# Performance work log

Hardware: AMD Instinct MI355X
Metric: run time of the kernel (lower is better)

The kernel has to match this reference:

```python
import jax, jax.numpy as jnp
import numpy as np

IH = IW = 1024          # image size (iH, iW)
NMS_CAND = 1000         # dup_attrs['nms_candidates']
NMS_THR = 0.65          # dup_attrs['nms_thr']
MAX_SEGS = 100          # max_segs


def _mask_to_box(masks):
    # masks: [N, H, W] bool -> xyxy float boxes [N, 4] in pixel coords
    N, H, W = masks.shape
    rows = masks.any(axis=2)            # [N, H]
    cols = masks.any(axis=1)            # [N, W]
    x1 = jnp.argmax(cols, axis=1)
    x2 = W - jnp.argmax(cols[:, ::-1], axis=1)
    y1 = jnp.argmax(rows, axis=1)
    y2 = H - jnp.argmax(rows[:, ::-1], axis=1)
    return jnp.stack([x1, y1, x2, y2], axis=-1).astype(jnp.float32)


def _box_iou(b):
    # b: [K, 4] xyxy -> pairwise IoU [K, K]
    x1, y1, x2, y2 = b[:, 0], b[:, 1], b[:, 2], b[:, 3]
    area = (x2 - x1) * (y2 - y1)
    ix1 = jnp.maximum(x1[:, None], x1[None, :])
    iy1 = jnp.maximum(y1[:, None], y1[None, :])
    ix2 = jnp.minimum(x2[:, None], x2[None, :])
    iy2 = jnp.minimum(y2[:, None], y2[None, :])
    inter = jnp.clip(ix2 - ix1, 0.0) * jnp.clip(iy2 - iy1, 0.0)
    union = area[:, None] + area[None, :] - inter
    return inter / jnp.maximum(union, 1e-9)


def _greedy_nms_keep(iou, thr):
    # boxes assumed pre-sorted by descending score; returns keep mask [K]
    k = iou.shape[0]
    idx = jnp.arange(k)

    def body(i, keep):
        sup = keep[i] & (iou[i] > thr) & (idx > i)
        return keep & ~sup

    return jax.lax.fori_loop(0, k, body, jnp.ones((k,), dtype=bool))


def setup_inputs() -> dict:
    key = jax.random.key(0)
    k1, k2 = jax.random.split(key)
    cls_logits = jax.random.normal(k1, (300, 81), dtype=jnp.float32)
    seg_logits = jax.random.normal(k2, (300, 200, 200), dtype=jnp.float32)
    return {"cls_logits": cls_logits, "seg_logits": seg_logits}


def reference(cls_logits, seg_logits):
    N, fH, fW = seg_logits.shape
    C = cls_logits.shape[1] - 1  # last class is background/no-object

    # mask thresholding + emptiness flag (filtering replaced by score masking)
    pred_masks = seg_logits > 0                              # [N, fH, fW]
    non_empty = pred_masks.reshape(N, -1).sum(axis=1) > 0    # [N]

    # mask -> box for NMS
    boxes = _mask_to_box(pred_masks)                         # [N, 4]

    # sigmoid scoring over (feat, class); empty masks get score -1 (never picked)
    scores = jax.nn.sigmoid(cls_logits[:, :-1])              # [N, C]
    scores = jnp.where(non_empty[:, None], scores, -1.0).reshape(-1)  # [N*C]
    feat_ids = jnp.repeat(jnp.arange(N), C)                  # [N*C]
    labels = jnp.tile(jnp.arange(C), N)                      # [N*C]

    # top nms_candidates (scores sorted descending)
    k = min(NMS_CAND, N * C)
    cand_scores, cand_ids = jax.lax.top_k(scores, k)
    cand_feats = feat_ids[cand_ids]
    cand_labels = labels[cand_ids]
    cand_boxes = boxes[cand_feats]

    # batched (class-aware) NMS: offset boxes per label
    offset = cand_labels.astype(jnp.float32)[:, None] * (float(max(fH, fW)) + 1.0)
    iou = _box_iou(cand_boxes + offset)
    keep = _greedy_nms_keep(iou, NMS_THR) & (cand_scores >= 0.0)

    # keep top max_segs among survivors
    kept_scores = jnp.where(keep, cand_scores, -jnp.inf)
    sel_scores, sel = jax.lax.top_k(kept_scores, MAX_SEGS)
    sel_feats = cand_feats[sel]
    sel_labels = cand_labels[sel]

    # upsample selected mask logits to image size and threshold
    sel_logits = seg_logits[sel_feats]                       # [M, fH, fW]
    maps = jax.image.resize(sel_logits, (MAX_SEGS, IH, IW), method='bilinear')
    out_masks = maps > 0                                     # [M, iH, iW] bool
    batch_ids = jnp.zeros((MAX_SEGS,), dtype=jnp.int32)

    return sel_labels, out_masks, sel_scores, batch_ids
```

## Files before the change

### kernel.cpp

```cpp
#include <hip/hip_runtime.h>
#include <cstdint>
#include <cstddef>

typedef unsigned int u32;
typedef unsigned long long u64;
typedef float vf4 __attribute__((ext_vector_type(4)));

#define NF 300
#define NCLS 80
#define NCLS1 81
#define FH 200
#define FW 200
#define PIX 40000
#define NC 24000
#define KCAND 1000
#define CAP 4096
#define NBINS 65536
#define MAXSEG 100
#define OUT_MASK_OFF 100
#define OUT_SCORE_OFF 104857700
#define OUT_BATCH_OFF 104857800
#define NEG_BIG -3.3895313892515355e38f
#define RYC 8

#define WS_HIST      0u
#define WS_KEYS      262144u
#define WS_COLLECT   454144u
#define WS_CNT       486912u
#define WS_BOXES     486928u
#define WS_CLAB      496928u
#define WS_CFEAT     500928u
#define WS_CSCORE    504928u
#define WS_CBOX      508928u
#define WS_ROWBITS   524928u
#define WS_SELFEAT   656128u
#define WS_WTAB      656528u

__device__ __forceinline__ u32 ord32_r3(float f) {
  u32 b = __float_as_uint(f);
  return (b & 0x80000000u) ? ~b : (b | 0x80000000u);
}
__device__ __forceinline__ float unord32_r3(u32 o) {
  u32 b = (o & 0x80000000u) ? (o & 0x7FFFFFFFu) : ~o;
  return __uint_as_float(b);
}

__global__ void r3_init_wtab(u32* __restrict__ hist, u32* __restrict__ cnts,
                             float4* __restrict__ wtab) {
  int i = blockIdx.x * 256 + threadIdx.x;
  hist[i] = 0u;
  if (i < 4) cnts[i] = 0u;
  if (i < 1024) {
    float s = __fsub_rn(__fmul_rn((float)i + 0.5f, 0.1953125f), 0.5f);
    int j0 = (int)floorf(s);
    int j1 = j0 + 1;
    float w0 = fmaxf(0.f, __fsub_rn(1.f, fabsf(__fsub_rn(s, (float)j0))));
    float w1 = fmaxf(0.f, __fsub_rn(1.f, fabsf(__fsub_rn(s, (float)j1))));
    bool in0 = (j0 >= 0) && (j0 < FH);
    bool in1 = (j1 >= 0) && (j1 < FH);
    float tot = __fadd_rn(in0 ? w0 : 0.f, in1 ? w1 : 0.f);
    float w0n = in0 ? (w0 / tot) : 0.f;
    float w1n = in1 ? (w1 / tot) : 0.f;
    wtab[i] = make_float4(w0n, w1n, (float)max(j0, 0), (float)min(j1, FH - 1));
  }
}

__global__ void r3_boxes_scores(const float* __restrict__ seg, const float* __restrict__ cls,
                                float4* __restrict__ boxes, u64* __restrict__ keys,
                                u32* __restrict__ hist) {
  __shared__ int sminx[256], sminy[256], smaxx[256], smaxy[256];
  int n = blockIdx.x, t = threadIdx.x;
  const float4* img = (const float4*)(seg + (size_t)n * PIX);
  int minx = FW, miny = FH, maxx = -1, maxy = -1;
  for (int q = t; q < PIX / 4; q += 256) {
    float4 v = img[q];
    int p = q * 4;
    int y = p / FW;
    int x = p - y * FW;
    if (v.x > 0.f) { minx = min(minx, x);     maxx = max(maxx, x);     miny = min(miny, y); maxy = max(maxy, y); }
    if (v.y > 0.f) { minx = min(minx, x + 1); maxx = max(maxx, x + 1); miny = min(miny, y); maxy = max(maxy, y); }
    if (v.z > 0.f) { minx = min(minx, x + 2); maxx = max(maxx, x + 2); miny = min(miny, y); maxy = max(maxy, y); }
    if (v.w > 0.f) { minx = min(minx, x + 3); maxx = max(maxx, x + 3); miny = min(miny, y); maxy = max(maxy, y); }
  }
  sminx[t] = minx; sminy[t] = miny; smaxx[t] = maxx; smaxy[t] = maxy;
  __syncthreads();
  for (int s = 128; s > 0; s >>= 1) {
    if (t < s) {
      sminx[t] = min(sminx[t], sminx[t + s]);
      sminy[t] = min(sminy[t], sminy[t + s]);
      smaxx[t] = max(smaxx[t], smaxx[t + s]);
      smaxy[t] = max(smaxy[t], smaxy[t + s]);
    }
    __syncthreads();
  }
  bool ne = smaxx[0] >= 0;
  if (t == 0) {
    float4 b;
    if (ne) b = make_float4((float)sminx[0], (float)sminy[0], (float)(smaxx[0] + 1), (float)(smaxy[0] + 1));
    else    b = make_float4(0.f, 0.f, (float)FW, (float)FH);
    boxes[n] = b;
  }
  if (t < NCLS) {
    float sc;
    if (ne) {
      float lg = cls[n * NCLS1 + t];
      sc = 1.0f / (1.0f + expf(-lg));
    } else {
      sc = -1.0f;
    }
    u32 o = ord32_r3(sc);
    u32 i = (u32)(n * NCLS + t);
    keys[i] = ((u64)o << 32) | (u64)(0xFFFFFFFFu - i);
    atomicAdd(&hist[o >> 16], 1u);
  }
}

__global__ void r3_thresh(const u32* __restrict__ hist, u32* __restrict__ cnts) {
  __shared__ u32 s[1024];
  int t = threadIdx.x;
  u32 sum = 0;
  const u32* hp = hist + t * 64;
  for (int b = 0; b < 64; b++) sum += hp[b];
  s[t] = sum;
  __syncthreads();
  for (int off = 1; off < 1024; off <<= 1) {
    u32 v = s[t];
    u32 o = (t + off < 1024) ? s[t + off] : 0u;
    __syncthreads();
    s[t] = v + o;
    __syncthreads();
  }
  u32 sufnext = (t < 1023) ? s[t + 1] : 0u;
  if (s[t] >= (u32)KCAND && sufnext < (u32)KCAND) {
    u32 run = sufnext;
    u32 B = (u32)(t * 64);
    for (int b = 63; b >= 0; b--) {
      run += hist[t * 64 + b];
      if (run >= (u32)KCAND) { B = (u32)(t * 64 + b); break; }
    }
    cnts[1] = B;
  }
}

__global__ void r3_collect(const u64* __restrict__ keys, const u32* __restrict__ cnts,
                           u64* __restrict__ collect, u32* __restrict__ counter) {
  int i = blockIdx.x * 256 + threadIdx.x;
  if (i >= NC) return;
  u64 k = keys[i];
  if ((u32)(k >> 48) >= cnts[1]) {
    u32 pos = atomicAdd(counter, 1u);
    if (pos < CAP) collect[pos] = k;
  }
}

__global__ void r3_rank(const u64* __restrict__ collect, const u32* __restrict__ cnts,
                        const float4* __restrict__ boxes,
                        int* __restrict__ clab, int* __restrict__ cfeat,
                        float* __restrict__ cscore, float4* __restrict__ cbox) {
  __shared__ u64 sk[CAP];
  int M = min((int)cnts[0], CAP);
  int t = threadIdx.x;
  for (int j = t; j < M; j += 64) sk[j] = collect[j];
  __syncthreads();
  for (int j = blockIdx.x * 64 + t; j < M; j += 64 * 16) {
    u64 mykey = sk[j];
    int r = 0;
    for (int k = 0; k < M; k++) r += (sk[k] > mykey) ? 1 : 0;
    if (r < KCAND) {
      u32 idx = 0xFFFFFFFFu - (u32)(mykey & 0xFFFFFFFFull);
      int n = (int)idx / NCLS, c = (int)idx - n * NCLS;
      clab[r] = c;
      cfeat[r] = n;
      cscore[r] = unord32_r3((u32)(mykey >> 32));
      float4 b = boxes[n];
      float off = (float)c * 201.0f;
      cbox[r] = make_float4(b.x + off, b.y + off, b.z + off, b.w + off);
    }
  }
}

__global__ void r3_iou(const float4* __restrict__ cbox, u64* __restrict__ rowbits) {
  int i = blockIdx.x;
  int lane = threadIdx.x;
  float4 bi = make_float4(0.f, 0.f, 0.f, 0.f);
  float ai = 0.f;
  if (i < KCAND) { bi = cbox[i]; ai = (bi.z - bi.x) * (bi.w - bi.y); }
  for (int ch = 0; ch < 16; ch++) {
    int j = ch * 64 + lane;
    bool pred = false;
    if (i < KCAND && j < KCAND && j > i) {
      float4 bj = cbox[j];
      float aj = (bj.z - bj.x) * (bj.w - bj.y);
      float ix1 = fmaxf(bi.x, bj.x), iy1 = fmaxf(bi.y, bj.y);
      float ix2 = fminf(bi.z, bj.z), iy2 = fminf(bi.w, bj.w);
      float inter = fmaxf(ix2 - ix1, 0.f) * fmaxf(iy2 - iy1, 0.f);
      float uni = ai + aj - inter;
      float iou = inter / fmaxf(uni, 1e-9f);
      pred = iou > 0.65f;
    }
    u64 m = __ballot(pred);
    if (lane == 0) rowbits[(size_t)i * 16 + ch] = m;
  }
}

__global__ void r3_nms_sel(const u64* __restrict__ rowbits, const float* __restrict__ cscore,
                           const int* __restrict__ clab, const int* __restrict__ cfeat,
                           float* __restrict__ out, int* __restrict__ selfeat) {
  __shared__ u64 sup[16];
  __shared__ u64 keep[16];
  __shared__ u64 sk[KCAND];
  int t = threadIdx.x;
  if (t < 16) sup[t] = 0ull;
  __syncthreads();
  for (int c = 0; c < 16; c++) {
    if (t < 64) {
      int L = t;
      u64 r = rowbits[(size_t)(c * 64 + L) * 16 + c];
      u64 s = sup[c];
      u64 k = 0ull;
      #pragma unroll 4
      for (int b = 0; b < 64; b++) {
        u64 rb = __shfl(r, b, 64);
        if (!((s >> b) & 1ull)) { s |= rb; k |= (1ull << b); }
      }
      if (L == 0) { sup[c] = s; keep[c] = k; }
      if (L > c && L < 16) {
        u64 acc = sup[L];
        for (int b = 0; b < 64; b++)
          if ((k >> b) & 1ull) acc |= rowbits[(size_t)(c * 64 + b) * 16 + L];
        sup[L] = acc;
      }
    }
    __syncthreads();
  }
  for (int j = t; j < KCAND; j += 1024) {
    bool kp = ((keep[j >> 6] >> (j & 63)) & 1ull) != 0ull;
    float sc = cscore[j];
    u32 hi = (kp && sc >= 0.f) ? ord32_r3(sc) : 0u;
    sk[j] = ((u64)hi << 32) | (u64)(0xFFFFFFFFu - (u32)j);
  }
  __syncthreads();
  if (t < KCAND) {
    u64 my = sk[t];
    int r = 0;
    for (int k = 0; k < KCAND; k++) r += (sk[k] > my) ? 1 : 0;
    if (r < MAXSEG) {
      u32 hi = (u32)(my >> 32);
      float oscore = (hi == 0u) ? NEG_BIG : unord32_r3(hi);
      oscore = fmaxf(oscore, NEG_BIG);
      out[r] = (float)clab[t];
      out[OUT_SCORE_OFF + r] = oscore;
      out[OUT_BATCH_OFF + r] = 0.0f;
      selfeat[r] = cfeat[t];
    }
  }
}

__global__ void __launch_bounds__(256) r3_resize(const float* __restrict__ seg,
                                                 const int* __restrict__ selfeat,
                                                 const float4* __restrict__ wtab,
                                                 float* __restrict__ outm) {
  __shared__ float4 swx[1024];
  __shared__ float srow[4][FW];
  int t = threadIdx.x;
  int yb = blockIdx.x * RYC, slot = blockIdx.y;
  int feat = selfeat[slot];
  const float* img = seg + (size_t)feat * PIX;
  #pragma unroll
  for (int k = 0; k < 4; k++) swx[t + 256 * k] = wtab[t + 256 * k];
  int ylo = (int)wtab[yb].z;
  int yhi = (int)wtab[yb + RYC - 1].w;
  int nr = yhi - ylo + 1;
  for (int e = t; e < nr * FW; e += 256) {
    int rr = e / FW, cc = e - rr * FW;
    srow[rr][cc] = img[(ylo + rr) * FW + cc];
  }
  __syncthreads();
  int xb = t * 4;
  float4 wxa = swx[xb], wxb = swx[xb + 1], wxc = swx[xb + 2], wxd = swx[xb + 3];
  int xa0 = (int)wxa.z, xa1 = (int)wxa.w;
  int xb0 = (int)wxb.z, xb1 = (int)wxb.w;
  int xc0 = (int)wxc.z, xc1 = (int)wxc.w;
  int xd0 = (int)wxd.z, xd1 = (int)wxd.w;
  float* obase = outm + (size_t)slot * 1048576 + (size_t)yb * 1024 + xb;
  #pragma unroll
  for (int r = 0; r < RYC; r++) {
    int y = yb + r;
    float4 wy = wtab[y];
    const float* r0 = srow[(int)wy.z - ylo];
    const float* r1 = srow[(int)wy.w - ylo];
    float wy0 = wy.x, wy1 = wy.y;
    float ta0 = __fmaf_rn(wy1, r1[xa0], __fmul_rn(wy0, r0[xa0]));
    float ta1 = __fmaf_rn(wy1, r1[xa1], __fmul_rn(wy0, r0[xa1]));
    float va  = __fmaf_rn(wxa.y, ta1, __fmul_rn(wxa.x, ta0));
    float tb0 = __fmaf_rn(wy1, r1[xb0], __fmul_rn(wy0, r0[xb0]));
    float tb1 = __fmaf_rn(wy1, r1[xb1], __fmul_rn(wy0, r0[xb1]));
    float vb  = __fmaf_rn(wxb.y, tb1, __fmul_rn(wxb.x, tb0));
    float tc0 = __fmaf_rn(wy1, r1[xc0], __fmul_rn(wy0, r0[xc0]));
    float tc1 = __fmaf_rn(wy1, r1[xc1], __fmul_rn(wy0, r0[xc1]));
    float vc  = __fmaf_rn(wxc.y, tc1, __fmul_rn(wxc.x, tc0));
    float td0 = __fmaf_rn(wy1, r1[xd0], __fmul_rn(wy0, r0[xd0]));
    float td1 = __fmaf_rn(wy1, r1[xd1], __fmul_rn(wy0, r0[xd1]));
    float vd  = __fmaf_rn(wxd.y, td1, __fmul_rn(wxd.x, td0));
    vf4 res;
    res.x = (va > 0.0f) ? 1.0f : 0.0f;
    res.y = (vb > 0.0f) ? 1.0f : 0.0f;
    res.z = (vc > 0.0f) ? 1.0f : 0.0f;
    res.w = (vd > 0.0f) ? 1.0f : 0.0f;
    __builtin_nontemporal_store(res, (vf4*)(obase + (size_t)r * 1024));
  }
}

extern "C" void kernel_launch(void* const* d_in, const int* in_sizes, int n_in,
                              void* d_out, int out_size, void* d_ws, size_t ws_size,
                              hipStream_t stream) {
  const float* cls = (const float*)d_in[0];
  const float* seg = (const float*)d_in[1];
  float* out = (float*)d_out;
  char* ws = (char*)d_ws;

  u32* hist      = (u32*)(ws + WS_HIST);
  u64* keys      = (u64*)(ws + WS_KEYS);
  u64* collect   = (u64*)(ws + WS_COLLECT);
  u32* cnts      = (u32*)(ws + WS_CNT);
  float4* boxes  = (float4*)(ws + WS_BOXES);
  int* clab      = (int*)(ws + WS_CLAB);
  int* cfeat     = (int*)(ws + WS_CFEAT);
  float* cscore  = (float*)(ws + WS_CSCORE);
  float4* cbox   = (float4*)(ws + WS_CBOX);
  u64* rowbits   = (u64*)(ws + WS_ROWBITS);
  int* selfeat   = (int*)(ws + WS_SELFEAT);
  float4* wtab   = (float4*)(ws + WS_WTAB);

  r3_init_wtab<<<dim3(NBINS / 256), dim3(256), 0, stream>>>(hist, cnts, wtab);
  r3_boxes_scores<<<dim3(NF), dim3(256), 0, stream>>>(seg, cls, boxes, keys, hist);
  r3_thresh<<<dim3(1), dim3(1024), 0, stream>>>(hist, cnts);
  r3_collect<<<dim3((NC + 255) / 256), dim3(256), 0, stream>>>(keys, cnts, collect, &cnts[0]);
  r3_rank<<<dim3(16), dim3(64), 0, stream>>>(collect, cnts, boxes, clab, cfeat, cscore, cbox);
  r3_iou<<<dim3(1024), dim3(64), 0, stream>>>(cbox, rowbits);
  r3_nms_sel<<<dim3(1), dim3(1024), 0, stream>>>(rowbits, cscore, clab, cfeat, out, selfeat);
  r3_resize<<<dim3(1024 / RYC, MAXSEG), dim3(256), 0, stream>>>(seg, selfeat, wtab, out + OUT_MASK_OFF);
}
```

Before: 648.7 us.

## Fuse init into boxes kernel and threshold with collect, use memset

```diff
diff --git a/kernel.cpp b/kernel.cpp
--- a/kernel.cpp
+++ b/kernel.cpp
@@ -36,21 +36,23 @@
 #define WS_SELFEAT   656128u
 #define WS_WTAB      656528u
 
-__device__ __forceinline__ u32 ord32_r3(float f) {
+__device__ __forceinline__ u32 ord32_r4(float f) {
   u32 b = __float_as_uint(f);
   return (b & 0x80000000u) ? ~b : (b | 0x80000000u);
 }
-__device__ __forceinline__ float unord32_r3(u32 o) {
+__device__ __forceinline__ float unord32_r4(u32 o) {
   u32 b = (o & 0x80000000u) ? (o & 0x7FFFFFFFu) : ~o;
   return __uint_as_float(b);
 }
 
-__global__ void r3_init_wtab(u32* __restrict__ hist, u32* __restrict__ cnts,
-                             float4* __restrict__ wtab) {
-  int i = blockIdx.x * 256 + threadIdx.x;
-  hist[i] = 0u;
-  if (i < 4) cnts[i] = 0u;
-  if (i < 1024) {
+__global__ void r4_boxes_scores(const float* __restrict__ seg, const float* __restrict__ cls,
+                                float4* __restrict__ boxes, u64* __restrict__ keys,
+                                u32* __restrict__ hist, float4* __restrict__ wtab) {
+  __shared__ int sminx[256], sminy[256], smaxx[256], smaxy[256];
+  int n = blockIdx.x, t = threadIdx.x;
+
+  if (n < 4) {
+    int i = n * 256 + t;
     float s = __fsub_rn(__fmul_rn((float)i + 0.5f, 0.1953125f), 0.5f);
     int j0 = (int)floorf(s);
     int j1 = j0 + 1;
@@ -63,17 +65,12 @@
     float w1n = in1 ? (w1 / tot) : 0.f;
     wtab[i] = make_float4(w0n, w1n, (float)max(j0, 0), (float)min(j1, FH - 1));
   }
-}
-
-__global__ void r3_boxes_scores(const float* __restrict__ seg, const float* __restrict__ cls,
-                                float4* __restrict__ boxes, u64* __restrict__ keys,
-                                u32* __restrict__ hist) {
-  __shared__ int sminx[256], sminy[256], smaxx[256], smaxy[256];
-  int n = blockIdx.x, t = threadIdx.x;
-  const float4* img = (const float4*)(seg + (size_t)n * PIX);
+
+  const vf4* img = (const vf4*)(seg + (size_t)n * PIX);
   int minx = FW, miny = FH, maxx = -1, maxy = -1;
+  #pragma unroll 4
   for (int q = t; q < PIX / 4; q += 256) {
-    float4 v = img[q];
+    vf4 v = __builtin_nontemporal_load(&img[q]);
     int p = q * 4;
     int y = p / FW;
     int x = p - y * FW;
@@ -108,19 +105,24 @@
     } else {
       sc = -1.0f;
     }
-    u32 o = ord32_r3(sc);
+    u32 o = ord32_r4(sc);
     u32 i = (u32)(n * NCLS + t);
     keys[i] = ((u64)o << 32) | (u64)(0xFFFFFFFFu - i);
     atomicAdd(&hist[o >> 16], 1u);
   }
 }
 
-__global__ void r3_thresh(const u32* __restrict__ hist, u32* __restrict__ cnts) {
+__global__ void r4_thresh_collect(const u32* __restrict__ hist, const u64* __restrict__ keys,
+                                  u64* __restrict__ collect, u32* __restrict__ cnts) {
   __shared__ u32 s[1024];
+  __shared__ u32 sB;
+  __shared__ u32 lcnt;
   int t = threadIdx.x;
+  if (t == 0) lcnt = 0u;
+  const uint4* hp = (const uint4*)(hist + t * 64);
   u32 sum = 0;
-  const u32* hp = hist + t * 64;
-  for (int b = 0; b < 64; b++) sum += hp[b];
+  #pragma unroll
+  for (int b = 0; b < 16; b++) { uint4 v = hp[b]; sum += v.x + v.y + v.z + v.w; }
   s[t] = sum;
   __syncthreads();
   for (int off = 1; off < 1024; off <<= 1) {
@@ -138,22 +140,22 @@
       run += hist[t * 64 + b];
       if (run >= (u32)KCAND) { B = (u32)(t * 64 + b); break; }
     }
-    cnts[1] = B;
-  }
-}
-
-__global__ void r3_collect(const u64* __restrict__ keys, const u32* __restrict__ cnts,
-                           u64* __restrict__ collect, u32* __restrict__ counter) {
-  int i = blockIdx.x * 256 + threadIdx.x;
-  if (i >= NC) return;
-  u64 k = keys[i];
-  if ((u32)(k >> 48) >= cnts[1]) {
-    u32 pos = atomicAdd(counter, 1u);
-    if (pos < CAP) collect[pos] = k;
-  }
-}
-
-__global__ void r3_rank(const u64* __restrict__ collect, const u32* __restrict__ cnts,
+    sB = B;
+  }
+  __syncthreads();
+  u32 B = sB;
+  for (int i = t; i < NC; i += 1024) {
+    u64 k = keys[i];
+    if ((u32)(k >> 48) >= B) {
+      u32 pos = atomicAdd(&lcnt, 1u);
+      if (pos < CAP) collect[pos] = k;
+    }
+  }
+  __syncthreads();
+  if (t == 0) cnts[0] = lcnt;
+}
+
+__global__ void r4_rank(const u64* __restrict__ collect, const u32* __restrict__ cnts,
                         const float4* __restrict__ boxes,
                         int* __restrict__ clab, int* __restrict__ cfeat,
                         float* __restrict__ cscore, float4* __restrict__ cbox) {
@@ -171,7 +173,7 @@
       int n = (int)idx / NCLS, c = (int)idx - n * NCLS;
       clab[r] = c;
       cfeat[r] = n;
-      cscore[r] = unord32_r3((u32)(mykey >> 32));
+      cscore[r] = unord32_r4((u32)(mykey >> 32));
       float4 b = boxes[n];
       float off = (float)c * 201.0f;
       cbox[r] = make_float4(b.x + off, b.y + off, b.z + off, b.w + off);
@@ -179,7 +181,7 @@
   }
 }
 
-__global__ void r3_iou(const float4* __restrict__ cbox, u64* __restrict__ rowbits) {
+__global__ void r4_iou(const float4* __restrict__ cbox, u64* __restrict__ rowbits) {
   int i = blockIdx.x;
   int lane = threadIdx.x;
   float4 bi = make_float4(0.f, 0.f, 0.f, 0.f);
@@ -203,7 +205,7 @@
   }
 }
 
-__global__ void r3_nms_sel(const u64* __restrict__ rowbits, const float* __restrict__ cscore,
+__global__ void r4_nms_sel(const u64* __restrict__ rowbits, const float* __restrict__ cscore,
                            const int* __restrict__ clab, const int* __restrict__ cfeat,
                            float* __restrict__ out, int* __restrict__ selfeat) {
   __shared__ u64 sup[16];
@@ -236,7 +238,7 @@
   for (int j = t; j < KCAND; j += 1024) {
     bool kp = ((keep[j >> 6] >> (j & 63)) & 1ull) != 0ull;
     float sc = cscore[j];
-    u32 hi = (kp && sc >= 0.f) ? ord32_r3(sc) : 0u;
+    u32 hi = (kp && sc >= 0.f) ? ord32_r4(sc) : 0u;
     sk[j] = ((u64)hi << 32) | (u64)(0xFFFFFFFFu - (u32)j);
   }
   __syncthreads();
@@ -246,7 +248,7 @@
     for (int k = 0; k < KCAND; k++) r += (sk[k] > my) ? 1 : 0;
     if (r < MAXSEG) {
       u32 hi = (u32)(my >> 32);
-      float oscore = (hi == 0u) ? NEG_BIG : unord32_r3(hi);
+      float oscore = (hi == 0u) ? NEG_BIG : unord32_r4(hi);
       oscore = fmaxf(oscore, NEG_BIG);
       out[r] = (float)clab[t];
       out[OUT_SCORE_OFF + r] = oscore;
@@ -256,7 +258,7 @@
   }
 }
 
-__global__ void __launch_bounds__(256) r3_resize(const float* __restrict__ seg,
+__global__ void __launch_bounds__(256) r4_resize(const float* __restrict__ seg,
                                                  const int* __restrict__ selfeat,
                                                  const float4* __restrict__ wtab,
                                                  float* __restrict__ outm) {
@@ -332,12 +334,11 @@
   int* selfeat   = (int*)(ws + WS_SELFEAT);
   float4* wtab   = (float4*)(ws + WS_WTAB);
 
-  r3_init_wtab<<<dim3(NBINS / 256), dim3(256), 0, stream>>>(hist, cnts, wtab);
-  r3_boxes_scores<<<dim3(NF), dim3(256), 0, stream>>>(seg, cls, boxes, keys, hist);
-  r3_thresh<<<dim3(1), dim3(1024), 0, stream>>>(hist, cnts);
-  r3_collect<<<dim3((NC + 255) / 256), dim3(256), 0, stream>>>(keys, cnts, collect, &cnts[0]);
-  r3_rank<<<dim3(16), dim3(64), 0, stream>>>(collect, cnts, boxes, clab, cfeat, cscore, cbox);
-  r3_iou<<<dim3(1024), dim3(64), 0, stream>>>(cbox, rowbits);
-  r3_nms_sel<<<dim3(1), dim3(1024), 0, stream>>>(rowbits, cscore, clab, cfeat, out, selfeat);
-  r3_resize<<<dim3(1024 / RYC, MAXSEG), dim3(256), 0, stream>>>(seg, selfeat, wtab, out + OUT_MASK_OFF);
-}
+  hipMemsetAsync(hist, 0, NBINS * sizeof(u32), stream);
+  r4_boxes_scores<<<dim3(NF), dim3(256), 0, stream>>>(seg, cls, boxes, keys, hist, wtab);
+  r4_thresh_collect<<<dim3(1), dim3(1024), 0, stream>>>(hist, keys, collect, cnts);
+  r4_rank<<<dim3(16), dim3(64), 0, stream>>>(collect, cnts, boxes, clab, cfeat, cscore, cbox);
+  r4_iou<<<dim3(1024), dim3(64), 0, stream>>>(cbox, rowbits);
+  r4_nms_sel<<<dim3(1), dim3(1024), 0, stream>>>(rowbits, cscore, clab, cfeat, out, selfeat);
+  r4_resize<<<dim3(1024 / RYC, MAXSEG), dim3(256), 0, stream>>>(seg, selfeat, wtab, out + OUT_MASK_OFF);
+}
```

Result: slower. 662.1 us (+2.1%).
